# Optimization experiments

Hardware: AMD Instinct MI355X
Metric: run time of the kernel (lower is better)

## Reference

```python
import jax, jax.numpy as jnp
import numpy as np


def setup_inputs() -> dict:
    key = jax.random.key(0)
    k1, k2 = jax.random.split(key)
    attn = jax.random.normal(k1, (2, 16, 1024, 4096), dtype=jnp.float32)
    ref_target_masks = jax.random.randint(k2, (4, 4096), 0, 2, dtype=jnp.int32)
    return {"attn": attn, "ref_target_masks": ref_target_masks}


def reference(attn, ref_target_masks):
    # mode = 'mean' (default in the torch module)
    masks = ref_target_masks.astype(attn.dtype)            # (C, R)
    sm = jax.nn.softmax(attn, axis=-1)                     # (B, H, S, R)
    # per-class masked sum over ref tokens: (C, B, H, S)
    weighted = jnp.einsum('bhsr,cr->cbhs', sm, masks)
    # normalize by mask sum per class
    weighted = weighted / masks.sum(axis=-1)[:, None, None, None]
    # permute (B,H,S)->(B,S,H) then mean over heads -> (C, B, S)
    return weighted.mean(axis=2)
```

## Files before the change

kernel.cpp:

```cpp
#include <hip/hip_runtime.h>

static constexpr int R = 4096;
static constexpr int C = 4;
static constexpr int NH = 16;
static constexpr int S = 1024;
static constexpr int B = 2;
static constexpr int BLOCK = 256;
static constexpr int NWAVE = BLOCK / 64;

__global__ __launch_bounds__(BLOCK) void pack_masks_kernel(
    const int* __restrict__ masks, unsigned char* __restrict__ codes,
    float* __restrict__ scale) {
  __shared__ float red[NWAVE][C];
  const int t = threadIdx.x;
  int cnt[C] = {0, 0, 0, 0};
  for (int k = 0; k < R / BLOCK; ++k) {
    const int r = k * BLOCK + t;
    unsigned code = 0;
#pragma unroll
    for (int c = 0; c < C; ++c) {
      const int m = (masks[c * R + r] != 0);
      code |= (unsigned)m << c;
      cnt[c] += m;
    }
    codes[r] = (unsigned char)code;
  }
#pragma unroll
  for (int c = 0; c < C; ++c) {
    float v = (float)cnt[c];
#pragma unroll
    for (int off = 32; off; off >>= 1) v += __shfl_xor(v, off, 64);
    if ((t & 63) == 0) red[t >> 6][c] = v;
  }
  __syncthreads();
  if (t == 0) {
#pragma unroll
    for (int c = 0; c < C; ++c) {
      float tot = 0.f;
      for (int w = 0; w < NWAVE; ++w) tot += red[w][c];
      scale[c] = 1.0f / (tot * (float)NH);
    }
  }
}

template <bool PACKED>
__global__ __launch_bounds__(BLOCK) void row_softmax_mask_kernel(
    const float* __restrict__ attn, const unsigned* __restrict__ codes,
    const float* __restrict__ scale, const int* __restrict__ masks,
    float* __restrict__ out) {
  const int row = blockIdx.x;
  const int t = threadIdx.x;

  __shared__ unsigned lds_words[PACKED ? 1 : (R / 4)];
  __shared__ float red[NWAVE][9];

  float cntf[C] = {0.f, 0.f, 0.f, 0.f};
  if constexpr (!PACKED) {
#pragma unroll
    for (int kw = 0; kw < R / 4 / BLOCK; ++kw) {
      const int j = kw * BLOCK + t;
      unsigned word = 0;
#pragma unroll
      for (int i = 0; i < 4; ++i) {
        const int r = 4 * j + i;
#pragma unroll
        for (int c = 0; c < C; ++c) {
          const int m = (masks[c * R + r] != 0);
          word |= (unsigned)m << (8 * i + c);
          cntf[c] += (float)m;
        }
      }
      lds_words[j] = word;
    }
    __syncthreads();
  }

  const float4* rowp = reinterpret_cast<const float4*>(attn + (size_t)row * R);
  float denom = 0.f;
  float num[C] = {0.f, 0.f, 0.f, 0.f};

#pragma unroll
  for (int k = 0; k < R / 4 / BLOCK; ++k) {
    const int j = k * BLOCK + t;
    const float4 a = rowp[j];
    const unsigned w = PACKED ? codes[j] : lds_words[j];
    const float av[4] = {a.x, a.y, a.z, a.w};
#pragma unroll
    for (int i = 0; i < 4; ++i) {
      const float e = __expf(av[i]);
      denom += e;
      const unsigned cc = w >> (8 * i);
#pragma unroll
      for (int c = 0; c < C; ++c) num[c] += ((cc >> c) & 1u) ? e : 0.f;
    }
  }

  const int NV = PACKED ? 5 : 9;
  float vals[9];
  vals[0] = denom;
#pragma unroll
  for (int c = 0; c < C; ++c) vals[1 + c] = num[c];
#pragma unroll
  for (int c = 0; c < C; ++c) vals[5 + c] = cntf[c];

#pragma unroll
  for (int iv = 0; iv < 9; ++iv) {
    if (iv >= NV) break;
    float v = vals[iv];
#pragma unroll
    for (int off = 32; off; off >>= 1) v += __shfl_xor(v, off, 64);
    vals[iv] = v;
  }
  const int wave = t >> 6;
  if ((t & 63) == 0) {
    for (int iv = 0; iv < NV; ++iv) red[wave][iv] = vals[iv];
  }
  __syncthreads();
  if (t == 0) {
    float tot[9];
    for (int iv = 0; iv < NV; ++iv)
      tot[iv] = red[0][iv] + red[1][iv] + red[2][iv] + red[3][iv];
    const float inv_d = 1.0f / tot[0];
    const int s = row & (S - 1);
    const int b = row >> 14;
    float* outp = out + b * S + s;
#pragma unroll
    for (int c = 0; c < C; ++c) {
      const float sc =
          PACKED ? scale[c] : (1.0f / (tot[5 + c] * (float)NH));
      atomicAdd(outp + c * (B * S), tot[1 + c] * inv_d * sc);
    }
  }
}

extern "C" void kernel_launch(void* const* d_in, const int* in_sizes, int n_in,
                              void* d_out, int out_size, void* d_ws,
                              size_t ws_size, hipStream_t stream) {
  const float* attn = (const float*)d_in[0];
  const int* masks = (const int*)d_in[1];
  float* out = (float*)d_out;

  hipMemsetAsync(d_out, 0, (size_t)out_size * sizeof(float), stream);

  const size_t need = (size_t)R + C * sizeof(float);
  if (ws_size >= need) {
    unsigned char* codes = (unsigned char*)d_ws;
    float* scale = (float*)((char*)d_ws + R);
    pack_masks_kernel<<<1, BLOCK, 0, stream>>>(masks, codes, scale);
    row_softmax_mask_kernel<true><<<B * NH * S, BLOCK, 0, stream>>>(
        attn, (const unsigned*)codes, scale, masks, out);
  } else {
    row_softmax_mask_kernel<false><<<B * NH * S, BLOCK, 0, stream>>>(
        attn, nullptr, nullptr, masks, out);
  }
}
```

Baseline: 676.4 us.

## Assign one wave per position over four heads with register-held mask codes

Replaces the one-block-per-row softmax kernel with a kernel where each 64-lane wave processes four heads for a single (batch, position). Mask codes are loaded once into registers and reused across the four heads. Reductions use only wave shuffles, and atomics are cut to one set per four rows. This removes LDS reductions and block barriers per row, at the cost of less intra-row parallelism and fewer threads in flight per row.

```diff
diff --git a/kernel.cpp b/kernel.cpp
--- a/kernel.cpp
+++ b/kernel.cpp
@@ -43,47 +43,101 @@
   }
 }
 
-template <bool PACKED>
-__global__ __launch_bounds__(BLOCK) void row_softmax_mask_kernel(
+__global__ __launch_bounds__(BLOCK, 4) void wave_rows_kernel(
     const float* __restrict__ attn, const unsigned* __restrict__ codes,
-    const float* __restrict__ scale, const int* __restrict__ masks,
+    const float* __restrict__ scale, float* __restrict__ out) {
+  const int t = threadIdx.x;
+  const int lane = t & 63;
+  const int wid = t >> 6;
+  const int wave = blockIdx.x * NWAVE + wid;
+  const int bs = wave >> 2;
+  const int hg = wave & 3;
+  const int b = bs >> 10;
+  const int s = bs & (S - 1);
+
+  unsigned cw[16];
+#pragma unroll
+  for (int i = 0; i < 16; ++i) cw[i] = codes[i * 64 + lane];
+
+  float res[C] = {0.f, 0.f, 0.f, 0.f};
+
+#pragma unroll
+  for (int hh = 0; hh < NH / 4; ++hh) {
+    const int h = hg * 4 + hh;
+    const size_t row = (size_t)(b * NH + h) * S + s;
+    const float4* rp = reinterpret_cast<const float4*>(attn + row * R);
+
+    float denom = 0.f;
+    float num[C] = {0.f, 0.f, 0.f, 0.f};
+#pragma unroll
+    for (int i = 0; i < 16; ++i) {
+      const float4 a = rp[i * 64 + lane];
+      const unsigned w = cw[i];
+      const float av[4] = {a.x, a.y, a.z, a.w};
+#pragma unroll
+      for (int e = 0; e < 4; ++e) {
+        const float ex = __expf(av[e]);
+        denom += ex;
+        const unsigned cc = w >> (8 * e);
+#pragma unroll
+        for (int c = 0; c < C; ++c) num[c] += ((cc >> c) & 1u) ? ex : 0.f;
+      }
+    }
+
+    float vals[5] = {denom, num[0], num[1], num[2], num[3]};
+#pragma unroll
+    for (int v = 0; v < 5; ++v) {
+#pragma unroll
+      for (int off = 32; off; off >>= 1) vals[v] += __shfl_xor(vals[v], off, 64);
+    }
+    const float invd = 1.0f / vals[0];
+#pragma unroll
+    for (int c = 0; c < C; ++c) res[c] += vals[1 + c] * invd;
+  }
+
+  if (lane == 0) {
+    float* outp = out + b * S + s;
+#pragma unroll
+    for (int c = 0; c < C; ++c)
+      atomicAdd(outp + c * (B * S), res[c] * scale[c]);
+  }
+}
+
+__global__ __launch_bounds__(BLOCK) void row_fallback_kernel(
+    const float* __restrict__ attn, const int* __restrict__ masks,
     float* __restrict__ out) {
   const int row = blockIdx.x;
   const int t = threadIdx.x;
-
-  __shared__ unsigned lds_words[PACKED ? 1 : (R / 4)];
+  __shared__ unsigned lds_words[R / 4];
   __shared__ float red[NWAVE][9];
 
   float cntf[C] = {0.f, 0.f, 0.f, 0.f};
-  if constexpr (!PACKED) {
 #pragma unroll
-    for (int kw = 0; kw < R / 4 / BLOCK; ++kw) {
-      const int j = kw * BLOCK + t;
-      unsigned word = 0;
+  for (int kw = 0; kw < R / 4 / BLOCK; ++kw) {
+    const int j = kw * BLOCK + t;
+    unsigned word = 0;
 #pragma unroll
-      for (int i = 0; i < 4; ++i) {
-        const int r = 4 * j + i;
+    for (int i = 0; i < 4; ++i) {
+      const int r = 4 * j + i;
 #pragma unroll
-        for (int c = 0; c < C; ++c) {
-          const int m = (masks[c * R + r] != 0);
-          word |= (unsigned)m << (8 * i + c);
-          cntf[c] += (float)m;
-        }
+      for (int c = 0; c < C; ++c) {
+        const int m = (masks[c * R + r] != 0);
+        word |= (unsigned)m << (8 * i + c);
+        cntf[c] += (float)m;
       }
-      lds_words[j] = word;
     }
-    __syncthreads();
+    lds_words[j] = word;
   }
+  __syncthreads();
 
   const float4* rowp = reinterpret_cast<const float4*>(attn + (size_t)row * R);
   float denom = 0.f;
   float num[C] = {0.f, 0.f, 0.f, 0.f};
-
 #pragma unroll
   for (int k = 0; k < R / 4 / BLOCK; ++k) {
     const int j = k * BLOCK + t;
     const float4 a = rowp[j];
-    const unsigned w = PACKED ? codes[j] : lds_words[j];
+    const unsigned w = lds_words[j];
     const float av[4] = {a.x, a.y, a.z, a.w};
 #pragma unroll
     for (int i = 0; i < 4; ++i) {
@@ -95,41 +149,29 @@
     }
   }
 
-  const int NV = PACKED ? 5 : 9;
-  float vals[9];
-  vals[0] = denom;
-#pragma unroll
-  for (int c = 0; c < C; ++c) vals[1 + c] = num[c];
-#pragma unroll
-  for (int c = 0; c < C; ++c) vals[5 + c] = cntf[c];
-
+  float vals[9] = {denom, num[0], num[1], num[2], num[3],
+                   cntf[0], cntf[1], cntf[2], cntf[3]};
 #pragma unroll
   for (int iv = 0; iv < 9; ++iv) {
-    if (iv >= NV) break;
-    float v = vals[iv];
 #pragma unroll
-    for (int off = 32; off; off >>= 1) v += __shfl_xor(v, off, 64);
-    vals[iv] = v;
+    for (int off = 32; off; off >>= 1) vals[iv] += __shfl_xor(vals[iv], off, 64);
   }
   const int wave = t >> 6;
-  if ((t & 63) == 0) {
-    for (int iv = 0; iv < NV; ++iv) red[wave][iv] = vals[iv];
-  }
+  if ((t & 63) == 0)
+    for (int iv = 0; iv < 9; ++iv) red[wave][iv] = vals[iv];
   __syncthreads();
   if (t == 0) {
     float tot[9];
-    for (int iv = 0; iv < NV; ++iv)
+    for (int iv = 0; iv < 9; ++iv)
       tot[iv] = red[0][iv] + red[1][iv] + red[2][iv] + red[3][iv];
     const float inv_d = 1.0f / tot[0];
     const int s = row & (S - 1);
     const int b = row >> 14;
     float* outp = out + b * S + s;
 #pragma unroll
-    for (int c = 0; c < C; ++c) {
-      const float sc =
-          PACKED ? scale[c] : (1.0f / (tot[5 + c] * (float)NH));
-      atomicAdd(outp + c * (B * S), tot[1 + c] * inv_d * sc);
-    }
+    for (int c = 0; c < C; ++c)
+      atomicAdd(outp + c * (B * S),
+                tot[1 + c] * inv_d / (tot[5 + c] * (float)NH));
   }
 }
 
@@ -147,10 +189,10 @@
     unsigned char* codes = (unsigned char*)d_ws;
     float* scale = (float*)((char*)d_ws + R);
     pack_masks_kernel<<<1, BLOCK, 0, stream>>>(masks, codes, scale);
-    row_softmax_mask_kernel<true><<<B * NH * S, BLOCK, 0, stream>>>(
-        attn, (const unsigned*)codes, scale, masks, out);
+    const int waves = B * S * 4;
+    wave_rows_kernel<<<waves / NWAVE, BLOCK, 0, stream>>>(
+        attn, (const unsigned*)codes, scale, out);
   } else {
-    row_softmax_mask_kernel<false><<<B * NH * S, BLOCK, 0, stream>>>(
-        attn, nullptr, nullptr, masks, out);
+    row_fallback_kernel<<<B * NH * S, BLOCK, 0, stream>>>(attn, masks, out);
   }
 }
```

New measurement: 709.3 us. 4.9% more time.
